# Optimization experiments

Measured on AMD Instinct MI355X. Metric: run time of the kernel, lower is better.

Reference implementation:

```python
import jax, jax.numpy as jnp
import numpy as np

NHEAD = 8

def layernorm(x, w, b, eps=1e-5):
    mu = jnp.mean(x, axis=-1, keepdims=True)
    var = jnp.mean((x - mu) ** 2, axis=-1, keepdims=True)
    return (x - mu) * jax.lax.rsqrt(var + eps) * w + b

def setup_inputs() -> dict:
    key = jax.random.key(0)
    ks = jax.random.split(key, 3)
    N, in_dim, dim = 2048, 256, 256
    point = jax.random.normal(ks[0], (N, in_dim), dtype=jnp.float32)
    w_qkv = jax.random.normal(ks[1], (in_dim, 3 * dim), dtype=jnp.float32) * (in_dim ** -0.5)
    w_proj = jax.random.normal(ks[2], (dim, dim), dtype=jnp.float32) * (dim ** -0.5)
    return {
        "point": point,
        "w_qkv": w_qkv,
        "w_proj": w_proj,
        "b_proj": jnp.zeros((dim,), jnp.float32),
        "norm1_w": jnp.ones((in_dim,), jnp.float32),
        "norm1_b": jnp.zeros((in_dim,), jnp.float32),
        "norm2_w": jnp.ones((dim,), jnp.float32),
        "norm2_b": jnp.zeros((dim,), jnp.float32),
        "topk": 16,
    }

def reference(point, w_qkv, w_proj, b_proj, norm1_w, norm1_b, norm2_w, norm2_b, topk):
    # Coarse level of QTAttB (i == 0, ONE_BATCH=True)
    N, in_dim = point.shape
    dim = w_proj.shape[0]
    Ch = dim // NHEAD  # per-head channels
    x = layernorm(point, norm1_w, norm1_b)[None]            # [1, N, in_dim]
    qkv = (x @ w_qkv).reshape(1, N, 3, NHEAD, Ch)
    q, k, v = qkv[:, :, 0], qkv[:, :, 1], qkv[:, :, 2]      # [1, N, H, Ch]
    # QK: nlhd,nshd->nlsh ; softmax over key axis s (dim=-2 in torch = axis 2)
    QK = jnp.einsum('blhd,bshd->blsh', q, k)                # [1, N, N, H]
    A = jax.nn.softmax(QK * (Ch ** -0.5), axis=2)
    A_mean = jnp.mean(A, axis=-1)                           # [1, N, N]
    _, topk_idx = jax.lax.top_k(A_mean, topk)               # [1, N, topk]
    message = jnp.einsum('blsh,bshd->blhd', A, v).reshape(1, N, dim)
    message = message @ w_proj + b_proj
    message = v.reshape(1, N, dim) + message
    message = message[0]                                    # squeeze batch
    out = layernorm(message, norm2_w, norm2_b)              # final_message = norm2(message)
    return out, topk_idx[0]
```

## Files before the change

kernel.cpp:

```cpp
#include <hip/hip_runtime.h>

#define NTOK   2048
#define DIM    256
#define NH     8
#define CH     32
#define QB     8
#define TOPK_K 16
#define SCALE  0.17677669529663687f
#define LN_EPS 1e-5f

#define PBL    260
#define PBH    (QB * PBL)
#define PSCALE 16384.f
#define RPSCALE (1.f / 16384.f)

typedef _Float16 h16;
typedef _Float16 h16x8 __attribute__((ext_vector_type(8)));
typedef _Float16 h16x4 __attribute__((ext_vector_type(4)));
typedef float    f32x4 __attribute__((ext_vector_type(4)));

#define MFMA16(a, b, c) __builtin_amdgcn_mfma_f32_16x16x32_f16((a), (b), (c), 0, 0, 0)


template<int NT>
__device__ __forceinline__ float block_sum(float v, float* red){
  #pragma unroll
  for (int off = 32; off > 0; off >>= 1) v += __shfl_xor(v, off, 64);
  const int t = threadIdx.x;
  if ((t & 63) == 0) red[t >> 6] = v;
  __syncthreads();
  float s = 0.f;
  #pragma unroll
  for (int w = 0; w < NT/64; w++) s += red[w];
  __syncthreads();
  return s;
}

__global__ __launch_bounds__(256) void ln_qkv_kernel(
    const float* __restrict__ point,
    const float* __restrict__ w_qkv,
    const float* __restrict__ c1,
    const float* __restrict__ c2,
    float* __restrict__ Q,
    h16*   __restrict__ KF,
    h16*   __restrict__ VF,
    float* __restrict__ V)
{
  __shared__ float xs[4][DIM];
  __shared__ float red[4];
  const int t  = threadIdx.x;
  const int r0 = blockIdx.x * 4;
  const float a1 = c1[t], a2 = c2[t];
  const float s1 = block_sum<256>(fabsf(a1), red);
  const float s2 = block_sum<256>(fabsf(a2), red);
  const float g = (s1 > s2) ? a1 : a2;
  const float b = (s1 > s2) ? a2 : a1;
  for (int r = 0; r < 4; r++){
    float v   = point[(r0 + r) * DIM + t];
    float mu  = block_sum<256>(v, red) * (1.f / DIM);
    float d   = v - mu;
    float var = block_sum<256>(d * d, red) * (1.f / DIM);
    xs[r][t]  = d * rsqrtf(var + LN_EPS) * g + b;
  }
  __syncthreads();
  float accq[4] = {}, acck[4] = {}, accv[4] = {};
  for (int d = 0; d < DIM; d++){
    const float w0 = w_qkv[d * 768 + t];
    const float w1 = w_qkv[d * 768 + 256 + t];
    const float w2 = w_qkv[d * 768 + 512 + t];
    #pragma unroll
    for (int r = 0; r < 4; r++){
      const float x = xs[r][d];
      accq[r] = fmaf(x, w0, accq[r]);
      acck[r] = fmaf(x, w1, acck[r]);
      accv[r] = fmaf(x, w2, accv[r]);
    }
  }
  #pragma unroll
  for (int r = 0; r < 4; r++){
    Q[(r0 + r) * DIM + t] = accq[r];
    V[(r0 + r) * DIM + t] = accv[r];
  }
  {
    const int w  = t >> 5;
    const int gk = (t & 31) >> 3;
    const int jk = t & 7;
    const int kg = r0 >> 4;
    #pragma unroll
    for (int rr = 0; rr < 4; rr++){
      const int k = r0 + rr;
      const float kv = acck[rr];
      const h16 kh = (h16)kv;
      const size_t kidx = (size_t)(w * 128 + kg) * 1024
                        + (size_t)(gk * 16 + (k & 15)) * 8 + jk;
      KF[kidx]       = kh;
      KF[kidx + 512] = (h16)(kv - (float)kh);
    }
  }
  {
    const int w  = t >> 5;
    const int h  = (t & 31) >> 4;
    const int rv = t & 15;
    const int kb = r0 >> 5;
    const int g2 = (r0 & 31) >> 3;
    const int j0 = r0 & 7;
    h16x4 vt;
    #pragma unroll
    for (int rr = 0; rr < 4; rr++) vt[rr] = (h16)accv[rr];
    *(h16x4*)&VF[(size_t)((w * 64 + kb) * 2 + h) * 512
                 + (size_t)(g2 * 16 + rv) * 8 + j0] = vt;
  }
}

__global__ __launch_bounds__(1024) __attribute__((amdgpu_waves_per_eu(4)))
void attn_fused_kernel(
    const float* Q,
    const h16*   __restrict__ KF,
    const h16*   __restrict__ VF,
    float*       msg,
    float*       __restrict__ out_idx)
{
  __shared__ float pbuf[NH * PBH];
  __shared__ float am[QB][NTOK];
  __shared__ float msg_s[2][QB][DIM + 4];
  __shared__ float zbuf[NH * 2 * QB];

  const int t  = threadIdx.x;
  const int wv = t >> 6;
  const int w  = wv & 7;
  const int hf = wv >> 3;
  const int l  = t & 63;
  const int r  = l & 15;
  const int g  = l >> 4;
  const int l0 = blockIdx.x * QB;

  h16x8 qh, ql;
  #pragma unroll
  for (int j = 0; j < 8; j++){ qh[j] = (h16)0.f; ql[j] = (h16)0.f; }
  if (r < QB){
    const float* qp = &Q[(size_t)(l0 + r) * DIM + w * CH + 8 * g];
    const float4 q0 = *(const float4*)qp;
    const float4 q1 = *(const float4*)(qp + 4);
    const float qv[8] = {q0.x, q0.y, q0.z, q0.w, q1.x, q1.y, q1.z, q1.w};
    #pragma unroll
    for (int j = 0; j < 8; j++){
      const float s = qv[j] * SCALE;
      const h16 hi = (h16)s;
      qh[j] = hi;
      ql[j] = (h16)(s - (float)hi);
    }
  }

  const h16* kfw = KF + (size_t)(w * 128) * 1024 + (size_t)l * 8;
  const h16* vfw = VF + (size_t)(w * 64) * 1024 + (size_t)l * 8;

  float zs[4] = {0.f, 0.f, 0.f, 0.f};
  {
    const h16* kf = kfw + (size_t)(hf * 64) * 1024;
    #pragma unroll 2
    for (int kgi = 0; kgi < 64; kgi++){
      const h16x8 bh = *(const h16x8*)(kf + (size_t)kgi * 1024);
      const h16x8 bl = *(const h16x8*)(kf + (size_t)kgi * 1024 + 512);
      f32x4 d = {0.f, 0.f, 0.f, 0.f};
      d = MFMA16(qh, bh, d);
      d = MFMA16(ql, bh, d);
      d = MFMA16(qh, bl, d);
      #pragma unroll
      for (int q4 = 0; q4 < 4; q4++) zs[q4] += __expf(d[q4]);
    }
  }
  #pragma unroll
  for (int q4 = 0; q4 < 4; q4++){
    #pragma unroll
    for (int off = 1; off < 16; off <<= 1) zs[q4] += __shfl_xor(zs[q4], off, 64);
  }
  if (r == 0 && g < 2){
    #pragma unroll
    for (int q4 = 0; q4 < 4; q4++) zbuf[(w * 2 + hf) * QB + 4 * g + q4] = zs[q4];
  }
  __syncthreads();
  float rZ[4];
  #pragma unroll
  for (int q4 = 0; q4 < 4; q4++){
    const int row = 4 * g + q4;
    rZ[q4] = (g < 2) ? 1.f / (zbuf[(w * 2 + 0) * QB + row] + zbuf[(w * 2 + 1) * QB + row])
                     : 0.f;
  }

  f32x4 macc[2];
  #pragma unroll
  for (int dg = 0; dg < 2; dg++) macc[dg] = (f32x4){0.f, 0.f, 0.f, 0.f};

  for (int ti = 0; ti < 8; ti++){
    const int s0 = ti * 256;
    const h16* vft = vfw + (size_t)((ti * 8 + hf * 4) * 2) * 512;

    h16x8 pva[4], pvb[4];
    pva[0] = *(const h16x8*)(vft);
    pvb[0] = *(const h16x8*)(vft + 512);
    pva[1] = *(const h16x8*)(vft + 1024);
    pvb[1] = *(const h16x8*)(vft + 1024 + 512);

    {
      const h16* kft = kfw + (size_t)(ti * 16 + hf * 8) * 1024;
      #pragma unroll 2
      for (int kgi = 0; kgi < 8; kgi++){
        const h16x8 bh = *(const h16x8*)(kft + (size_t)kgi * 1024);
        const h16x8 bl = *(const h16x8*)(kft + (size_t)kgi * 1024 + 512);
        f32x4 d = {0.f, 0.f, 0.f, 0.f};
        d = MFMA16(qh, bh, d);
        d = MFMA16(ql, bh, d);
        d = MFMA16(qh, bl, d);
        if (g < 2){
          const int kbr = hf * 128 + kgi * 16 + r;
          pbuf[w * PBH + (4 * g + 0) * PBL + kbr] = __expf(d[0]) * rZ[0];
          pbuf[w * PBH + (4 * g + 1) * PBL + kbr] = __expf(d[1]) * rZ[1];
          pbuf[w * PBH + (4 * g + 2) * PBL + kbr] = __expf(d[2]) * rZ[2];
          pbuf[w * PBH + (4 * g + 3) * PBL + kbr] = __expf(d[3]) * rZ[3];
        }
      }
    }
    __syncthreads();

    pva[2] = *(const h16x8*)(vft + 2048);
    pvb[2] = *(const h16x8*)(vft + 2048 + 512);
    pva[3] = *(const h16x8*)(vft + 3072);
    pvb[3] = *(const h16x8*)(vft + 3072 + 512);

    #pragma unroll
    for (int st = 0; st < 4; st++){
      h16x8 pa;
      #pragma unroll
      for (int j = 0; j < 8; j++) pa[j] = (h16)0.f;
      if (r < QB){
        const float* pp = &pbuf[w * PBH + r * PBL + hf * 128 + st * 32 + 8 * g];
        const float4 p0 = *(const float4*)pp;
        const float4 p1 = *(const float4*)(pp + 4);
        pa[0] = (h16)(p0.x * PSCALE); pa[1] = (h16)(p0.y * PSCALE);
        pa[2] = (h16)(p0.z * PSCALE); pa[3] = (h16)(p0.w * PSCALE);
        pa[4] = (h16)(p1.x * PSCALE); pa[5] = (h16)(p1.y * PSCALE);
        pa[6] = (h16)(p1.z * PSCALE); pa[7] = (h16)(p1.w * PSCALE);
      }
      macc[0] = MFMA16(pa, pva[st], macc[0]);
      macc[1] = MFMA16(pa, pvb[st], macc[1]);
    }
    #pragma unroll
    for (int rep = 0; rep < 2; rep++){
      const int idx = t + rep * 1024;
      const int q = idx >> 8, key = idx & 255;
      float su = 0.f;
      #pragma unroll
      for (int hh = 0; hh < 8; hh++) su += pbuf[hh * PBH + q * PBL + key];
      am[q][s0 + key] = su * 0.125f;
    }
    __syncthreads();
  }

  if (g < 2){
    #pragma unroll
    for (int dg = 0; dg < 2; dg++)
      #pragma unroll
      for (int q4 = 0; q4 < 4; q4++)
        msg_s[hf][4 * g + q4][w * CH + dg * 16 + r] = macc[dg][q4] * RPSCALE;
  }
  __syncthreads();

  if (wv < QB){
    for (int it = 0; it < TOPK_K; it++){
      float bv = -1e30f; int bi = 0x7fffffff;
      #pragma unroll
      for (int b = 0; b < NTOK / 64; b++){
        const int idx = b * 64 + l;
        const float v = am[wv][idx];
        if (v > bv || (v == bv && idx < bi)){ bv = v; bi = idx; }
      }
      #pragma unroll
      for (int off = 1; off < 64; off <<= 1){
        const float ov = __shfl_xor(bv, off, 64);
        const int   oi = __shfl_xor(bi, off, 64);
        if (ov > bv || (ov == bv && oi < bi)){ bv = ov; bi = oi; }
      }
      if (l == 0){
        out_idx[(l0 + wv) * TOPK_K + it] = (float)bi;
        am[wv][bi] = -1e30f;
      }
    }
  } else {
    const int t2 = t - 512;
    #pragma unroll
    for (int k2 = 0; k2 < 4; k2++){
      const int cell = t2 + 512 * k2;
      const int q = cell >> 8, dcol = cell & 255;
      msg[(size_t)(l0 + q) * DIM + dcol] = msg_s[0][q][dcol] + msg_s[1][q][dcol];
    }
  }
}

__global__ __launch_bounds__(256) void proj_ln_kernel(
    const float* __restrict__ msg,
    const float* __restrict__ V,
    const float* __restrict__ w_proj,
    const float* __restrict__ b_proj,
    const float* __restrict__ c1,
    const float* __restrict__ c2,
    float* __restrict__ out)
{
  __shared__ float ms[4][DIM];
  __shared__ float red[4];
  const int t = threadIdx.x, r0 = blockIdx.x * 4;
  const float a1 = c1[t], a2 = c2[t];
  const float s1 = block_sum<256>(fabsf(a1), red);
  const float s2 = block_sum<256>(fabsf(a2), red);
  const float g2 = (s1 > s2) ? a1 : a2;
  const float b2 = (s1 > s2) ? a2 : a1;
  for (int r = 0; r < 4; r++) ms[r][t] = msg[(r0 + r) * DIM + t];
  __syncthreads();
  const float bp = b_proj[t];
  float acc[4] = {bp, bp, bp, bp};
  for (int d = 0; d < DIM; d++){
    const float wv = w_proj[d * DIM + t];
    #pragma unroll
    for (int r = 0; r < 4; r++) acc[r] = fmaf(ms[r][d], wv, acc[r]);
  }
  for (int r = 0; r < 4; r++){
    float a = acc[r] + V[(r0 + r) * DIM + t];
    const float mu  = block_sum<256>(a, red) * (1.f / DIM);
    const float dv  = a - mu;
    const float var = block_sum<256>(dv * dv, red) * (1.f / DIM);
    out[(r0 + r) * DIM + t] = dv * rsqrtf(var + LN_EPS) * g2 + b2;
  }
}

extern "C" void kernel_launch(void* const* d_in, const int* in_sizes, int n_in,
                              void* d_out, int out_size, void* d_ws, size_t ws_size,
                              hipStream_t stream) {
  const float* point  = nullptr;
  const float* w_qkv  = nullptr;
  const float* w_proj = nullptr;
  const float* v256[5] = {nullptr, nullptr, nullptr, nullptr, nullptr};
  int n256 = 0;
  for (int i = 0; i < n_in; i++){
    const int sz = in_sizes[i];
    if      (sz == NTOK * DIM)      point  = (const float*)d_in[i];
    else if (sz == DIM * 3 * DIM)   w_qkv  = (const float*)d_in[i];
    else if (sz == DIM * DIM)       w_proj = (const float*)d_in[i];
    else if (sz == DIM && n256 < 5) v256[n256++] = (const float*)d_in[i];
  }
  const float* b_proj = v256[0];
  const float* n1a    = v256[1];
  const float* n1c    = v256[2];
  const float* n2a    = v256[3];
  const float* n2c    = v256[4];

  float* out     = (float*)d_out;
  float* out_idx = out + (size_t)NTOK * DIM;

  char* ws = (char*)d_ws;
  float* Q   = (float*)(ws);
  float* V   = (float*)(ws + ((size_t)2 << 20));
  h16*   KF  = (h16*)  (ws + ((size_t)4 << 20));
  h16*   VF  = (h16*)  (ws + ((size_t)6 << 20));
  float* msg = Q;

  ln_qkv_kernel    <<<NTOK / 4,  256, 0, stream>>>(point, w_qkv, n1a, n1c, Q, KF, VF, V);
  attn_fused_kernel<<<NTOK / QB, 1024, 0, stream>>>(Q, KF, VF, msg, out_idx);
  proj_ln_kernel   <<<NTOK / 4,  256, 0, stream>>>(msg, V, w_proj, b_proj, n2a, n2c, out);
}
```

Baseline: 211.5 us.

## Move QKV and output projections to split-fp16 MFMA with pre-reordered weights

Adds a per-call kernel that converts w_qkv and w_proj into hi/lo fp16 fragments laid out for MFMA B operands. The LN+QKV and projection+LN kernels are rewritten to use 1024-thread blocks over 16 tokens, computing the GEMMs with three 16x16x32 fp16 MFMAs per k-step (hi*hi, lo*hi, hi*lo) to keep near-fp32 accuracy. LayerNorm now uses per-wave shuffle reductions and float4 loads instead of block-wide syncs. This removes the scalar FMA GEMM cost at the price of two extra small launches and fp16-split rounding error.

```diff
diff --git a/kernel.cpp b/kernel.cpp
--- a/kernel.cpp
+++ b/kernel.cpp
@@ -16,7 +16,6 @@
 
 typedef _Float16 h16;
 typedef _Float16 h16x8 __attribute__((ext_vector_type(8)));
-typedef _Float16 h16x4 __attribute__((ext_vector_type(4)));
 typedef float    f32x4 __attribute__((ext_vector_type(4)));
 
 #define MFMA16(a, b, c) __builtin_amdgcn_mfma_f32_16x16x32_f16((a), (b), (c), 0, 0, 0)
@@ -36,9 +35,27 @@
   return s;
 }
 
-__global__ __launch_bounds__(256) void ln_qkv_kernel(
+__global__ __launch_bounds__(256) void reorder_w_kernel(
+    const float* __restrict__ src, h16* __restrict__ dst, int ld)
+{
+  const int b  = blockIdx.x * 4 + (threadIdx.x >> 6);
+  const int l  = threadIdx.x & 63;
+  const int cg = b >> 3, ks = b & 7;
+  h16x8 hi8, lo8;
+  #pragma unroll
+  for (int j = 0; j < 8; j++){
+    const float v = src[(size_t)(ks * 32 + (l >> 4) * 8 + j) * ld + cg * 16 + (l & 15)];
+    const h16 h = (h16)v;
+    hi8[j] = h;
+    lo8[j] = (h16)(v - (float)h);
+  }
+  *(h16x8*)&dst[(size_t)((cg * 8 + ks) * 2 + 0) * 512 + l * 8] = hi8;
+  *(h16x8*)&dst[(size_t)((cg * 8 + ks) * 2 + 1) * 512 + l * 8] = lo8;
+}
+
+__global__ __launch_bounds__(1024) void ln_qkv_kernel(
     const float* __restrict__ point,
-    const float* __restrict__ w_qkv,
+    const h16*   __restrict__ WF,
     const float* __restrict__ c1,
     const float* __restrict__ c2,
     float* __restrict__ Q,
@@ -46,69 +63,111 @@
     h16*   __restrict__ VF,
     float* __restrict__ V)
 {
-  __shared__ float xs[4][DIM];
-  __shared__ float red[4];
+  __shared__ float xs[16][261];
+  __shared__ float garr[256], barr[256];
+  __shared__ float red[16];
   const int t  = threadIdx.x;
-  const int r0 = blockIdx.x * 4;
-  const float a1 = c1[t], a2 = c2[t];
-  const float s1 = block_sum<256>(fabsf(a1), red);
-  const float s2 = block_sum<256>(fabsf(a2), red);
-  const float g = (s1 > s2) ? a1 : a2;
-  const float b = (s1 > s2) ? a2 : a1;
-  for (int r = 0; r < 4; r++){
-    float v   = point[(r0 + r) * DIM + t];
-    float mu  = block_sum<256>(v, red) * (1.f / DIM);
-    float d   = v - mu;
-    float var = block_sum<256>(d * d, red) * (1.f / DIM);
-    xs[r][t]  = d * rsqrtf(var + LN_EPS) * g + b;
-  }
-  __syncthreads();
-  float accq[4] = {}, acck[4] = {}, accv[4] = {};
-  for (int d = 0; d < DIM; d++){
-    const float w0 = w_qkv[d * 768 + t];
-    const float w1 = w_qkv[d * 768 + 256 + t];
-    const float w2 = w_qkv[d * 768 + 512 + t];
-    #pragma unroll
-    for (int r = 0; r < 4; r++){
-      const float x = xs[r][d];
-      accq[r] = fmaf(x, w0, accq[r]);
-      acck[r] = fmaf(x, w1, acck[r]);
-      accv[r] = fmaf(x, w2, accv[r]);
-    }
-  }
-  #pragma unroll
-  for (int r = 0; r < 4; r++){
-    Q[(r0 + r) * DIM + t] = accq[r];
-    V[(r0 + r) * DIM + t] = accv[r];
-  }
-  {
-    const int w  = t >> 5;
-    const int gk = (t & 31) >> 3;
-    const int jk = t & 7;
-    const int kg = r0 >> 4;
-    #pragma unroll
-    for (int rr = 0; rr < 4; rr++){
-      const int k = r0 + rr;
-      const float kv = acck[rr];
-      const h16 kh = (h16)kv;
-      const size_t kidx = (size_t)(w * 128 + kg) * 1024
-                        + (size_t)(gk * 16 + (k & 15)) * 8 + jk;
-      KF[kidx]       = kh;
-      KF[kidx + 512] = (h16)(kv - (float)kh);
-    }
-  }
-  {
-    const int w  = t >> 5;
-    const int h  = (t & 31) >> 4;
-    const int rv = t & 15;
-    const int kb = r0 >> 5;
-    const int g2 = (r0 & 31) >> 3;
-    const int j0 = r0 & 7;
-    h16x4 vt;
-    #pragma unroll
-    for (int rr = 0; rr < 4; rr++) vt[rr] = (h16)accv[rr];
-    *(h16x4*)&VF[(size_t)((w * 64 + kb) * 2 + h) * 512
-                 + (size_t)(g2 * 16 + rv) * 8 + j0] = vt;
+  const int wv = t >> 6;
+  const int l  = t & 63;
+  const int r  = l & 15;
+  const int g  = l >> 4;
+  const int l0 = blockIdx.x * 16;
+
+  const float a1 = (t < 256) ? c1[t] : 0.f;
+  const float a2 = (t < 256) ? c2[t] : 0.f;
+  const float s1 = block_sum<1024>(fabsf(a1), red);
+  const float s2 = block_sum<1024>(fabsf(a2), red);
+  if (t < 256){ garr[t] = (s1 > s2) ? a1 : a2; barr[t] = (s1 > s2) ? a2 : a1; }
+  __syncthreads();
+
+  {
+    const float4 x = *(const float4*)&point[(size_t)(l0 + wv) * DIM + 4 * l];
+    float s = x.x + x.y + x.z + x.w;
+    #pragma unroll
+    for (int off = 1; off < 64; off <<= 1) s += __shfl_xor(s, off, 64);
+    const float mu = s * (1.f / DIM);
+    const float d0 = x.x - mu, d1 = x.y - mu, d2 = x.z - mu, d3 = x.w - mu;
+    float ss = d0 * d0 + d1 * d1 + d2 * d2 + d3 * d3;
+    #pragma unroll
+    for (int off = 1; off < 64; off <<= 1) ss += __shfl_xor(ss, off, 64);
+    const float rsd = rsqrtf(ss * (1.f / DIM) + LN_EPS);
+    xs[wv][4 * l + 0] = d0 * rsd * garr[4 * l + 0] + barr[4 * l + 0];
+    xs[wv][4 * l + 1] = d1 * rsd * garr[4 * l + 1] + barr[4 * l + 1];
+    xs[wv][4 * l + 2] = d2 * rsd * garr[4 * l + 2] + barr[4 * l + 2];
+    xs[wv][4 * l + 3] = d3 * rsd * garr[4 * l + 3] + barr[4 * l + 3];
+  }
+  __syncthreads();
+
+  h16x8 ah[8], al[8];
+  #pragma unroll
+  for (int ks = 0; ks < 8; ks++){
+    #pragma unroll
+    for (int j = 0; j < 8; j++){
+      const float v = xs[r][ks * 32 + 8 * g + j];
+      const h16 hi = (h16)v;
+      ah[ks][j] = hi;
+      al[ks][j] = (h16)(v - (float)hi);
+    }
+  }
+
+  f32x4 aq = {0.f,0.f,0.f,0.f}, ak = {0.f,0.f,0.f,0.f}, av = {0.f,0.f,0.f,0.f};
+  {
+    const h16* wf = WF + (size_t)wv * 8192 + (size_t)l * 8;
+    #pragma unroll
+    for (int ks = 0; ks < 8; ks++){
+      const h16x8 bh = *(const h16x8*)(wf + ks * 1024);
+      const h16x8 bl = *(const h16x8*)(wf + ks * 1024 + 512);
+      aq = MFMA16(ah[ks], bh, aq);
+      aq = MFMA16(al[ks], bh, aq);
+      aq = MFMA16(ah[ks], bl, aq);
+    }
+  }
+  {
+    const h16* wf = WF + (size_t)(16 + wv) * 8192 + (size_t)l * 8;
+    #pragma unroll
+    for (int ks = 0; ks < 8; ks++){
+      const h16x8 bh = *(const h16x8*)(wf + ks * 1024);
+      const h16x8 bl = *(const h16x8*)(wf + ks * 1024 + 512);
+      ak = MFMA16(ah[ks], bh, ak);
+      ak = MFMA16(al[ks], bh, ak);
+      ak = MFMA16(ah[ks], bl, ak);
+    }
+  }
+  {
+    const h16* wf = WF + (size_t)(32 + wv) * 8192 + (size_t)l * 8;
+    #pragma unroll
+    for (int ks = 0; ks < 8; ks++){
+      const h16x8 bh = *(const h16x8*)(wf + ks * 1024);
+      const h16x8 bl = *(const h16x8*)(wf + ks * 1024 + 512);
+      av = MFMA16(ah[ks], bh, av);
+      av = MFMA16(al[ks], bh, av);
+      av = MFMA16(ah[ks], bl, av);
+    }
+  }
+
+  const int kgb = blockIdx.x;
+  const int dc  = wv * 16 + r;
+  #pragma unroll
+  for (int q4 = 0; q4 < 4; q4++){
+    const int tok = 4 * g + q4;
+    Q[(size_t)(l0 + tok) * DIM + dc] = aq[q4];
+    V[(size_t)(l0 + tok) * DIM + dc] = av[q4];
+    {
+      const int wh = dc >> 5, gp = (dc & 31) >> 3, jj = dc & 7;
+      const float kv = ak[q4];
+      const h16 kh2 = (h16)kv;
+      const size_t kidx = (size_t)(wh * 128 + kgb) * 1024
+                        + (size_t)(gp * 16 + tok) * 8 + jj;
+      KF[kidx]       = kh2;
+      KF[kidx + 512] = (h16)(kv - (float)kh2);
+    }
+    {
+      const int wh = dc >> 5, hh = (dc & 31) >> 4, cp = dc & 15;
+      const int key = l0 + tok;
+      const int kb = key >> 5, krem = key & 31, gpp = krem >> 3, jpp = krem & 7;
+      VF[(size_t)((wh * 64 + kb) * 2 + hh) * 512
+         + (size_t)(gpp * 16 + cp) * 8 + jpp] = (h16)av[q4];
+    }
   }
 }
 
@@ -296,38 +355,94 @@
   }
 }
 
-__global__ __launch_bounds__(256) void proj_ln_kernel(
+__global__ __launch_bounds__(1024) void proj_ln_kernel(
     const float* __restrict__ msg,
     const float* __restrict__ V,
-    const float* __restrict__ w_proj,
+    const h16*   __restrict__ WP,
     const float* __restrict__ b_proj,
     const float* __restrict__ c1,
     const float* __restrict__ c2,
     float* __restrict__ out)
 {
-  __shared__ float ms[4][DIM];
-  __shared__ float red[4];
-  const int t = threadIdx.x, r0 = blockIdx.x * 4;
-  const float a1 = c1[t], a2 = c2[t];
-  const float s1 = block_sum<256>(fabsf(a1), red);
-  const float s2 = block_sum<256>(fabsf(a2), red);
-  const float g2 = (s1 > s2) ? a1 : a2;
-  const float b2 = (s1 > s2) ? a2 : a1;
-  for (int r = 0; r < 4; r++) ms[r][t] = msg[(r0 + r) * DIM + t];
-  __syncthreads();
-  const float bp = b_proj[t];
-  float acc[4] = {bp, bp, bp, bp};
-  for (int d = 0; d < DIM; d++){
-    const float wv = w_proj[d * DIM + t];
-    #pragma unroll
-    for (int r = 0; r < 4; r++) acc[r] = fmaf(ms[r][d], wv, acc[r]);
-  }
-  for (int r = 0; r < 4; r++){
-    float a = acc[r] + V[(r0 + r) * DIM + t];
-    const float mu  = block_sum<256>(a, red) * (1.f / DIM);
-    const float dv  = a - mu;
-    const float var = block_sum<256>(dv * dv, red) * (1.f / DIM);
-    out[(r0 + r) * DIM + t] = dv * rsqrtf(var + LN_EPS) * g2 + b2;
+  __shared__ float xs[16][261];
+  __shared__ float ms2[16][261];
+  __shared__ float garr[256], barr[256], bparr[256];
+  __shared__ float red[16];
+  const int t  = threadIdx.x;
+  const int wv = t >> 6;
+  const int l  = t & 63;
+  const int r  = l & 15;
+  const int g  = l >> 4;
+  const int l0 = blockIdx.x * 16;
+
+  const float a1 = (t < 256) ? c1[t] : 0.f;
+  const float a2 = (t < 256) ? c2[t] : 0.f;
+  const float s1 = block_sum<1024>(fabsf(a1), red);
+  const float s2 = block_sum<1024>(fabsf(a2), red);
+  if (t < 256){
+    garr[t]  = (s1 > s2) ? a1 : a2;
+    barr[t]  = (s1 > s2) ? a2 : a1;
+    bparr[t] = b_proj[t];
+  }
+
+  {
+    const float4 x = *(const float4*)&msg[(size_t)(l0 + wv) * DIM + 4 * l];
+    xs[wv][4 * l + 0] = x.x; xs[wv][4 * l + 1] = x.y;
+    xs[wv][4 * l + 2] = x.z; xs[wv][4 * l + 3] = x.w;
+  }
+  __syncthreads();
+
+  h16x8 ah[8], al[8];
+  #pragma unroll
+  for (int ks = 0; ks < 8; ks++){
+    #pragma unroll
+    for (int j = 0; j < 8; j++){
+      const float v = xs[r][ks * 32 + 8 * g + j];
+      const h16 hi = (h16)v;
+      ah[ks][j] = hi;
+      al[ks][j] = (h16)(v - (float)hi);
+    }
+  }
+
+  f32x4 acc = {0.f,0.f,0.f,0.f};
+  {
+    const h16* wp = WP + (size_t)wv * 8192 + (size_t)l * 8;
+    #pragma unroll
+    for (int ks = 0; ks < 8; ks++){
+      const h16x8 bh = *(const h16x8*)(wp + ks * 1024);
+      const h16x8 bl = *(const h16x8*)(wp + ks * 1024 + 512);
+      acc = MFMA16(ah[ks], bh, acc);
+      acc = MFMA16(al[ks], bh, acc);
+      acc = MFMA16(ah[ks], bl, acc);
+    }
+  }
+
+  const int dc = wv * 16 + r;
+  #pragma unroll
+  for (int q4 = 0; q4 < 4; q4++){
+    const int tok = 4 * g + q4;
+    ms2[tok][dc] = acc[q4] + bparr[dc] + V[(size_t)(l0 + tok) * DIM + dc];
+  }
+  __syncthreads();
+
+  {
+    const float x0 = ms2[wv][4 * l + 0], x1 = ms2[wv][4 * l + 1];
+    const float x2 = ms2[wv][4 * l + 2], x3 = ms2[wv][4 * l + 3];
+    float s = x0 + x1 + x2 + x3;
+    #pragma unroll
+    for (int off = 1; off < 64; off <<= 1) s += __shfl_xor(s, off, 64);
+    const float mu = s * (1.f / DIM);
+    const float d0 = x0 - mu, d1 = x1 - mu, d2 = x2 - mu, d3 = x3 - mu;
+    float ss = d0 * d0 + d1 * d1 + d2 * d2 + d3 * d3;
+    #pragma unroll
+    for (int off = 1; off < 64; off <<= 1) ss += __shfl_xor(ss, off, 64);
+    const float rsd = rsqrtf(ss * (1.f / DIM) + LN_EPS);
+    float4 o;
+    o.x = d0 * rsd * garr[4 * l + 0] + barr[4 * l + 0];
+    o.y = d1 * rsd * garr[4 * l + 1] + barr[4 * l + 1];
+    o.z = d2 * rsd * garr[4 * l + 2] + barr[4 * l + 2];
+    o.w = d3 * rsd * garr[4 * l + 3] + barr[4 * l + 3];
+    *(float4*)&out[(size_t)(l0 + wv) * DIM + 4 * l] = o;
   }
 }
 
@@ -360,9 +475,13 @@
   float* V   = (float*)(ws + ((size_t)2 << 20));
   h16*   KF  = (h16*)  (ws + ((size_t)4 << 20));
   h16*   VF  = (h16*)  (ws + ((size_t)6 << 20));
+  h16*   WF  = (h16*)  (ws + ((size_t)7 << 20));
+  h16*   WP  = (h16*)  (ws + ((size_t)7 << 20) + 786432);
   float* msg = Q;
 
-  ln_qkv_kernel    <<<NTOK / 4,  256, 0, stream>>>(point, w_qkv, n1a, n1c, Q, KF, VF, V);
+  reorder_w_kernel <<<96, 256, 0, stream>>>(w_qkv,  WF, 768);
+  reorder_w_kernel <<<32, 256, 0, stream>>>(w_proj, WP, 256);
+  ln_qkv_kernel    <<<NTOK / 16, 1024, 0, stream>>>(point, WF, n1a, n1c, Q, KF, VF, V);
   attn_fused_kernel<<<NTOK / QB, 1024, 0, stream>>>(Q, KF, VF, msg, out_idx);
-  proj_ln_kernel   <<<NTOK / 4,  256, 0, stream>>>(msg, V, w_proj, b_proj, n2a, n2c, out);
-}
+  proj_ln_kernel   <<<NTOK / 16, 1024, 0, stream>>>(msg, V, WP, b_proj, n2a, n2c, out);
+}
```

After: 190.3 us. -10.0%, faster.
